# Optimization experiments

Measured on AMD Instinct MI355X. Metric: run time of the kernel, lower is better.

Reference implementation:

```python
import jax, jax.numpy as jnp
import numpy as np

BS, T, FIN, FOUT = 8, 1024, 512, 512
ALPHA = 0.1      # leaky relu slope
T_K = 3          # t_ksize (odd); temporal band radius = T_K // 2
S_K = 4          # s_ksize semantic topk
NEG_INF = -9e15


def setup_inputs() -> dict:
    key = jax.random.key(0)
    k1, k2, k3, k4 = jax.random.split(key, 4)
    # xavier-uniform-ish scales (gain 1.414)
    w_lim = 1.414 * np.sqrt(6.0 / (FIN + FOUT))
    a_lim = 1.414 * np.sqrt(6.0 / (2 * FOUT + 1))
    return {
        "x_a": jax.random.normal(k1, (BS, T, FIN), jnp.float32),
        "x_v": jax.random.normal(k2, (BS, T, FIN), jnp.float32),
        "W": jax.random.uniform(k3, (FIN, FOUT), jnp.float32, -w_lim, w_lim),
        "a": jax.random.uniform(k4, (2 * FOUT, 1), jnp.float32, -a_lim, a_lim),
    }


def _temporal_mask(t):
    # tem_adj[i,j] = 1 iff |i-j| <= T_K//2 and i, j on the same side of t-0.5
    idx = jnp.arange(2 * t)
    same_side = (idx[:, None] >= t) == (idx[None, :] >= t)
    band = jnp.abs(idx[:, None] - idx[None, :]) <= (T_K // 2)
    return band & same_side  # (2t, 2t) bool


def _semantic_block_mask(x, k):
    # x: (bs, t, d). Top-k neighbors by negative squared euclidean distance.
    inner = 2.0 * jnp.einsum("btd,bsd->bts", x, x)
    sq = jnp.sum(x * x, axis=-1, keepdims=True)  # (bs, t, 1)
    pd = -(sq - inner + jnp.swapaxes(sq, -1, -2))  # (bs, t, t)
    _, idx = jax.lax.top_k(pd, k)  # (bs, t, k)
    bs, t = x.shape[0], x.shape[1]
    b_ix = jnp.arange(bs)[:, None, None]
    r_ix = jnp.arange(t)[None, :, None]
    return jnp.zeros((bs, t, t), bool).at[b_ix, r_ix, idx].set(True)


def reference(x_a, x_v, W, a):
    bs, t, _ = x_a.shape
    h = jnp.concatenate([x_a, x_v], axis=1)          # (bs, 2t, FIN)
    Wh = h @ W                                        # (bs, 2t, FOUT)

    # additive GAT score: e = leakyrelu(Wh a1 + (Wh a2)^T)
    Wh1 = Wh @ a[:FOUT]                               # (bs, 2t, 1)
    Wh2 = Wh @ a[FOUT:]                               # (bs, 2t, 1)
    e = Wh1 + jnp.swapaxes(Wh2, -1, -2)               # (bs, 2t, 2t)
    e = jnp.where(e > 0, e, ALPHA * e)                # leaky relu

    # adjacency: temporal band + semantic topk within aa / vv blocks
    tem = _temporal_mask(t)                           # (2t, 2t)
    sem_aa = _semantic_block_mask(Wh[:, :t], S_K)     # (bs, t, t)
    sem_vv = _semantic_block_mask(Wh[:, t:], S_K)     # (bs, t, t)
    zb = jnp.zeros((bs, t, t), bool)
    sem = jnp.concatenate([
        jnp.concatenate([sem_aa, zb], axis=-1),
        jnp.concatenate([zb, sem_vv], axis=-1),
    ], axis=1)                                        # (bs, 2t, 2t)
    mask = tem[None] | sem

    attention = jax.nn.softmax(jnp.where(mask, e, NEG_INF), axis=-1)
    h_prime = jax.nn.elu(attention @ Wh)              # (bs, 2t, FOUT)
    return h_prime[:, :t], h_prime[:, t:]
```

## Files before the change

### kernel.cpp

```cpp
#include <hip/hip_runtime.h>
#include <math.h>

#define T_ 1024
#define BS_ 8
#define D_ 512
#define NROWS_ (BS_*2*T_)
#define ALPHA_ 0.1f

typedef _Float16 f16;
typedef _Float16 f16x8 __attribute__((ext_vector_type(8)));
typedef _Float16 f16x4 __attribute__((ext_vector_type(4)));
typedef float f32x4 __attribute__((ext_vector_type(4)));

#define MFMA16(A,B,C) __builtin_amdgcn_mfma_f32_16x16x32_f16((A),(B),(C),0,0,0)

__device__ __forceinline__ void gl16(const void* g, void* l) {
    __builtin_amdgcn_global_load_lds(
        (const __attribute__((address_space(1))) unsigned int*)g,
        (__attribute__((address_space(3))) unsigned int*)l, 16, 0, 0);
}

__device__ __forceinline__ unsigned sortable(float f) {
    unsigned u = __float_as_uint(f);
    return u ^ ((u & 0x80000000u) ? 0xFFFFFFFFu : 0x80000000u);
}
__device__ __forceinline__ unsigned pack_key(float s, int col) {
    return (sortable(s) & 0xFFFFFC00u) | (unsigned)(1023 - col);
}

#define INSK4(K, X) { \
    bool g3 = (X) > K[3], g2 = (X) > K[2], g1 = (X) > K[1], g0 = (X) > K[0]; \
    K[3] = g2 ? K[2] : (g3 ? (X) : K[3]); \
    K[2] = g1 ? K[1] : (g2 ? (X) : K[2]); \
    K[1] = g0 ? K[0] : (g1 ? (X) : K[1]); \
    K[0] = g0 ? (X) : K[0]; }

#define INSK8(K, X) { \
    bool h7=(X)>K[7],h6=(X)>K[6],h5=(X)>K[5],h4=(X)>K[4]; \
    bool h3=(X)>K[3],h2=(X)>K[2],h1=(X)>K[1],h0=(X)>K[0]; \
    K[7]=h6?K[6]:(h7?(X):K[7]); K[6]=h5?K[5]:(h6?(X):K[6]); \
    K[5]=h4?K[4]:(h5?(X):K[5]); K[4]=h3?K[3]:(h4?(X):K[4]); \
    K[3]=h2?K[2]:(h3?(X):K[3]); K[2]=h1?K[1]:(h2?(X):K[2]); \
    K[1]=h0?K[0]:(h1?(X):K[1]); K[0]=h0?(X):K[0]; }

#define CEU(a,b) { unsigned mx_ = (a) > (b) ? (a) : (b); \
    unsigned mn_ = (a) > (b) ? (b) : (a); (a) = mx_; (b) = mn_; }

#define MERGE8(K, MSK) { \
    unsigned b0=__shfl_xor(K[0],MSK), b1=__shfl_xor(K[1],MSK), \
             b2=__shfl_xor(K[2],MSK), b3=__shfl_xor(K[3],MSK), \
             b4=__shfl_xor(K[4],MSK), b5=__shfl_xor(K[5],MSK), \
             b6=__shfl_xor(K[6],MSK), b7=__shfl_xor(K[7],MSK); \
    K[0]=K[0]>b7?K[0]:b7; K[1]=K[1]>b6?K[1]:b6; \
    K[2]=K[2]>b5?K[2]:b5; K[3]=K[3]>b4?K[3]:b4; \
    K[4]=K[4]>b3?K[4]:b3; K[5]=K[5]>b2?K[5]:b2; \
    K[6]=K[6]>b1?K[6]:b1; K[7]=K[7]>b0?K[7]:b0; \
    CEU(K[0],K[4]); CEU(K[1],K[5]); CEU(K[2],K[6]); CEU(K[3],K[7]); \
    CEU(K[0],K[2]); CEU(K[1],K[3]); CEU(K[4],K[6]); CEU(K[5],K[7]); \
    CEU(K[0],K[1]); CEU(K[2],K[3]); CEU(K[4],K[5]); CEU(K[6],K[7]); }

#define BETTER(x,xi,v,vi) ((x) > (v) || ((x) == (v) && (xi) < (vi)))
#define INS4T(TV,TI,X,ID) { \
    bool g3 = BETTER(X,ID,TV[3],TI[3]), g2 = BETTER(X,ID,TV[2],TI[2]); \
    bool g1 = BETTER(X,ID,TV[1],TI[1]), g0 = BETTER(X,ID,TV[0],TI[0]); \
    TV[3] = g2 ? TV[2] : (g3 ? (X) : TV[3]); TI[3] = g2 ? TI[2] : (g3 ? (ID) : TI[3]); \
    TV[2] = g1 ? TV[1] : (g2 ? (X) : TV[2]); TI[2] = g1 ? TI[1] : (g2 ? (ID) : TI[2]); \
    TV[1] = g0 ? TV[0] : (g1 ? (X) : TV[1]); TI[1] = g0 ? TI[0] : (g1 ? (ID) : TI[1]); \
    TV[0] = g0 ? (X) : TV[0]; TI[0] = g0 ? (ID) : TI[0]; }

__global__ __launch_bounds__(256) void k_splitW(
    const float* __restrict__ W, f16* __restrict__ WTh, f16* __restrict__ WTl)
{
    __shared__ float tile[64][65];
    const int tid = threadIdx.x;
    const int tk = (blockIdx.x >> 3) << 6, tn = (blockIdx.x & 7) << 6;
    const int r0 = tid >> 4, c4 = (tid & 15) << 2;

    #pragma unroll
    for (int rr = 0; rr < 4; ++rr) {
        int k = r0 + (rr << 4);
        float4 v = *(const float4*)(W + (size_t)(tk + k) * D_ + tn + c4);
        tile[k][c4+0] = v.x; tile[k][c4+1] = v.y;
        tile[k][c4+2] = v.z; tile[k][c4+3] = v.w;
    }
    __syncthreads();
    #pragma unroll
    for (int rr = 0; rr < 4; ++rr) {
        int n = r0 + (rr << 4);
        f16x4 h, l;
        #pragma unroll
        for (int i = 0; i < 4; ++i) {
            float x = tile[c4 + i][n];
            f16 hh = (f16)x; h[i] = hh; l[i] = (f16)(x - (float)hh);
        }
        *(f16x4*)(WTh + (size_t)(tn + n) * D_ + tk + c4) = h;
        *(f16x4*)(WTl + (size_t)(tn + n) * D_ + tk + c4) = l;
    }
}

__global__ __launch_bounds__(512, 2) void k_gemm_wh(
    const float* __restrict__ xa, const float* __restrict__ xv,
    const f16* __restrict__ WTh, const f16* __restrict__ WTl,
    const float* __restrict__ a,
    f16* __restrict__ Whh, f16* __restrict__ Whl,
    float* __restrict__ Wh1, float* __restrict__ Wh2, float* __restrict__ sq)
{
    __shared__ __align__(16) unsigned char smem[135168];

    const int tid  = threadIdx.x;
    const int w    = tid >> 6;
    const int wr   = w >> 2, wc = w & 3;
    const int lane = tid & 63;
    const int l15  = lane & 15;
    const int g    = lane >> 4;
    const int r8   = lane >> 3;
    const int k7   = lane & 7;
    const int sw2  = ((k7 ^ r8) << 4);
    const int q0x  = ((g ^ (lane & 7)) << 4);
    const int rowbase = blockIdx.x << 6;

    if (tid < 256)
        *(float4*)(smem + 131072 + (tid << 4)) = *(const float4*)(a + (tid << 2));

    const int qp = rowbase >> 10;
    const float* xsrc = ((qp & 1) ? xv : xa)
                      + (size_t)((qp >> 1) * 1024 + (rowbase & 1023)) * D_;
    const int arow = (wr << 5) + l15;

    const char* WThB = (const char*)WTh;
    const char* WTlB = (const char*)WTl;

    const int bo0 = (((wc << 6) +  0 + l15) << 7) + q0x;
    const int bo1 = (((wc << 6) + 16 + l15) << 7) + q0x;
    const int bo2 = (((wc << 6) + 32 + l15) << 7) + q0x;
    const int bo3 = (((wc << 6) + 48 + l15) << 7) + q0x;

    #define STAGE_B(ct_, kc_, buf_) { \
        size_t gB_ = ((size_t)(((ct_) << 8) + (w << 5) + r8) << 10) + ((kc_) << 7) + sw2; \
        int ldsB_ = (buf_) * 65536 + (w << 12) + (lane << 4); \
        _Pragma("unroll") \
        for (int j_ = 0; j_ < 4; ++j_) { \
            gl16(WThB + gB_, smem + ldsB_); \
            gl16(WTlB + gB_, smem + 32768 + ldsB_); \
            gB_ += (size_t)8 << 10; ldsB_ += 1024; } }

    #define LOAD_A(dst_, kc_) { \
        _Pragma("unroll") \
        for (int r_ = 0; r_ < 2; ++r_) { \
            const float* p_ = xsrc + (size_t)(arow + (r_ << 4)) * D_ + ((kc_) << 6) + (g << 3); \
            dst_[(r_ << 2) + 0] = *(const float4*)(p_); \
            dst_[(r_ << 2) + 1] = *(const float4*)(p_ + 4); \
            dst_[(r_ << 2) + 2] = *(const float4*)(p_ + 32); \
            dst_[(r_ << 2) + 3] = *(const float4*)(p_ + 36); } }

    #define CONV_A(src_) { \
        _Pragma("unroll") \
        for (int r_ = 0; r_ < 2; ++r_) \
        _Pragma("unroll") \
        for (int s_ = 0; s_ < 2; ++s_) { \
            float4 v0_ = src_[(r_ << 2) + (s_ << 1)]; \
            float4 v1_ = src_[(r_ << 2) + (s_ << 1) + 1]; \
            float xs_[8] = {v0_.x,v0_.y,v0_.z,v0_.w,v1_.x,v1_.y,v1_.z,v1_.w}; \
            f16x8 h_, l_; \
            _Pragma("unroll") \
            for (int e_ = 0; e_ < 8; ++e_) { \
                f16 hh_ = (f16)xs_[e_]; h_[e_] = hh_; l_[e_] = (f16)(xs_[e_] - (float)hh_); } \
            AH[r_][s_] = h_; AL[r_][s_] = l_; } }

    f32x4 acc[2][2][4];
    #pragma unroll
    for (int ct = 0; ct < 2; ++ct)
        #pragma unroll
        for (int m = 0; m < 2; ++m)
            #pragma unroll
            for (int c = 0; c < 4; ++c) acc[ct][m][c] = (f32x4){0.f,0.f,0.f,0.f};

    float4 aR[8];
    f16x8 AH[2][2], AL[2][2];

    LOAD_A(aR, 0);
    STAGE_B(0, 0, 0);

    #pragma unroll
    for (int t = 0; t < 16; ++t) {
        const int kc = t >> 1, ct = t & 1, bufb = (t & 1) * 65536;
        __syncthreads();
        if (t < 15) STAGE_B((t + 1) & 1, (t + 1) >> 1, (t + 1) & 1);
        if (ct == 0) { CONV_A(aR); }
        else if (kc < 7) { LOAD_A(aR, kc + 1); }

        #pragma unroll
        for (int s = 0; s < 2; ++s) {
            const int sx = s << 6;
            f16x8 bh0 = *(const f16x8*)(smem + bufb + (bo0 ^ sx));
            f16x8 bh1 = *(const f16x8*)(smem + bufb + (bo1 ^ sx));
            f16x8 bh2 = *(const f16x8*)(smem + bufb + (bo2 ^ sx));
            f16x8 bh3 = *(const f16x8*)(smem + bufb + (bo3 ^ sx));
            f16x8 bl0 = *(const f16x8*)(smem + bufb + 32768 + (bo0 ^ sx));
            f16x8 bl1 = *(const f16x8*)(smem + bufb + 32768 + (bo1 ^ sx));
            f16x8 bl2 = *(const f16x8*)(smem + bufb + 32768 + (bo2 ^ sx));
            f16x8 bl3 = *(const f16x8*)(smem + bufb + 32768 + (bo3 ^ sx));

            acc[ct][0][0] = MFMA16(AH[0][s], bh0, acc[ct][0][0]);
            acc[ct][0][1] = MFMA16(AH[0][s], bh1, acc[ct][0][1]);
            acc[ct][0][2] = MFMA16(AH[0][s], bh2, acc[ct][0][2]);
            acc[ct][0][3] = MFMA16(AH[0][s], bh3, acc[ct][0][3]);
            acc[ct][1][0] = MFMA16(AH[1][s], bh0, acc[ct][1][0]);
            acc[ct][1][1] = MFMA16(AH[1][s], bh1, acc[ct][1][1]);
            acc[ct][1][2] = MFMA16(AH[1][s], bh2, acc[ct][1][2]);
            acc[ct][1][3] = MFMA16(AH[1][s], bh3, acc[ct][1][3]);
            acc[ct][0][0] = MFMA16(AL[0][s], bh0, acc[ct][0][0]);
            acc[ct][0][1] = MFMA16(AL[0][s], bh1, acc[ct][0][1]);
            acc[ct][0][2] = MFMA16(AL[0][s], bh2, acc[ct][0][2]);
            acc[ct][0][3] = MFMA16(AL[0][s], bh3, acc[ct][0][3]);
            acc[ct][1][0] = MFMA16(AL[1][s], bh0, acc[ct][1][0]);
            acc[ct][1][1] = MFMA16(AL[1][s], bh1, acc[ct][1][1]);
            acc[ct][1][2] = MFMA16(AL[1][s], bh2, acc[ct][1][2]);
            acc[ct][1][3] = MFMA16(AL[1][s], bh3, acc[ct][1][3]);
            acc[ct][0][0] = MFMA16(AH[0][s], bl0, acc[ct][0][0]);
            acc[ct][0][1] = MFMA16(AH[0][s], bl1, acc[ct][0][1]);
            acc[ct][0][2] = MFMA16(AH[0][s], bl2, acc[ct][0][2]);
            acc[ct][0][3] = MFMA16(AH[0][s], bl3, acc[ct][0][3]);
            acc[ct][1][0] = MFMA16(AH[1][s], bl0, acc[ct][1][0]);
            acc[ct][1][1] = MFMA16(AH[1][s], bl1, acc[ct][1][1]);
            acc[ct][1][2] = MFMA16(AH[1][s], bl2, acc[ct][1][2]);
            acc[ct][1][3] = MFMA16(AH[1][s], bl3, acc[ct][1][3]);
        }
    }
    #undef STAGE_B
    #undef LOAD_A
    #undef CONV_A

    __syncthreads();

    float st1[8], st2[8], stq[8];
    #pragma unroll
    for (int s = 0; s < 8; ++s) { st1[s] = 0.f; st2[s] = 0.f; stq[s] = 0.f; }

    #pragma unroll
    for (int ct = 0; ct < 2; ++ct)
        #pragma unroll
        for (int c = 0; c < 4; ++c) {
            const int col = (ct << 8) + (wc << 6) + (c << 4) + l15;
            const float a1 = *(const float*)(smem + 131072 + (col << 2));
            const float a2 = *(const float*)(smem + 131072 + 2048 + (col << 2));
            #pragma unroll
            for (int m = 0; m < 2; ++m)
                #pragma unroll
                for (int j = 0; j < 4; ++j) {
                    const float v = acc[ct][m][c][j];
                    const int slot = (m << 2) + j;
                    st1[slot] = fmaf(v, a1, st1[slot]);
                    st2[slot] = fmaf(v, a2, st2[slot]);
                    stq[slot] = fmaf(v, v,  stq[slot]);
                    f16 h = (f16)v; f16 l = (f16)(v - (float)h);
                    const size_t off = (size_t)(rowbase + (wr << 5) + (m << 4) + (g << 2) + j) * D_ + col;
                    Whh[off] = h; Whl[off] = l;
                }
        }

    #pragma unroll
    for (int mask = 1; mask < 16; mask <<= 1)
        #pragma unroll
        for (int s = 0; s < 8; ++s) {
            st1[s] += __shfl_xor(st1[s], mask);
            st2[s] += __shfl_xor(st2[s], mask);
            stq[s] += __shfl_xor(stq[s], mask);
        }
    if (l15 == 0) {
        #pragma unroll
        for (int s = 0; s < 8; ++s) {
            const int rl = (wr << 5) + ((s >> 2) << 4) + (g << 2) + (s & 3);
            float* sp = (float*)smem + ((rl << 2) + wc) * 3;
            sp[0] = st1[s]; sp[1] = st2[s]; sp[2] = stq[s];
        }
    }
    __syncthreads();
    if (tid < 64) {
        float s1 = 0.f, s2 = 0.f, s3 = 0.f;
        #pragma unroll
        for (int wv = 0; wv < 4; ++wv) {
            const float* sp = (const float*)smem + ((tid << 2) + wv) * 3;
            s1 += sp[0]; s2 += sp[1]; s3 += sp[2];
        }
        Wh1[rowbase + tid] = s1; Wh2[rowbase + tid] = s2; sq[rowbase + tid] = s3;
    }
}

__global__ __launch_bounds__(512, 1) void k_gram_topk8(
    const f16* __restrict__ Whh, const float* __restrict__ sq,
    int* __restrict__ topk8)
{
    __shared__ __align__(16) unsigned char smem[81920];

    const int bid = blockIdx.x;
    const int swz = ((bid & 7) << 5) + (bid >> 3);
    const int p   = swz >> 4;
    const int rt  = swz & 15;
    const int rowbase  = (p << 10) + (rt << 6);
    const int colPanel = p << 10;

    const int tid  = threadIdx.x;
    const int w    = tid >> 6;
    const int wr   = w >> 2, wc = w & 3;
    const int lane = tid & 63;
    const int l15  = lane & 15;
    const int g    = lane >> 4;
    const int r8   = lane >> 3;
    const int k7   = lane & 7;
    const int sw2  = ((k7 ^ r8) << 4);
    const int q0x  = ((g ^ (lane & 7)) << 4);

    const int rowA = tid >> 3;
    const int k7A  = tid & 7;
    const int aswz = ((k7A ^ (rowA & 7)) << 4);

    const char* WB = (const char*)Whh;

    const int aoff0 = 32768 + (((wr << 5) +  0 + l15) << 7) + q0x;
    const int aoff1 = 32768 + (((wr << 5) + 16 + l15) << 7) + q0x;
    const int boff0 = (((wc << 6) +  0 + l15) << 7) + q0x;
    const int boff1 = (((wc << 6) + 16 + l15) << 7) + q0x;
    const int boff2 = (((wc << 6) + 32 + l15) << 7) + q0x;
    const int boff3 = (((wc << 6) + 48 + l15) << 7) + q0x;

    f32x4 acc[2][4];
    #pragma unroll
    for (int m = 0; m < 2; ++m)
        #pragma unroll
        for (int c = 0; c < 4; ++c) acc[m][c] = (f32x4){0.f,0.f,0.f,0.f};

    unsigned k4[8][4];
    #pragma unroll
    for (int s = 0; s < 8; ++s)
        #pragma unroll
        for (int q = 0; q < 4; ++q) k4[s][q] = 0u;

    #define STAGE_G(t) { \
        const int ct_ = (t) >> 3, kc_ = (t) & 7; \
        const int bufb_ = ((t) & 1) * 40960; \
        size_t gB_ = ((size_t)(colPanel + (ct_ << 8) + (w << 5) + r8) << 10) + (kc_ << 7) + sw2; \
        int ldsB_ = bufb_ + (w << 12) + (lane << 4); \
        _Pragma("unroll") \
        for (int j_ = 0; j_ < 4; ++j_) { \
            gl16(WB + gB_, smem + ldsB_); \
            gB_ += (size_t)8 << 10; ldsB_ += 1024; \
        } \
        size_t gA_ = ((size_t)(rowbase + rowA) << 10) + (kc_ << 7) + aswz; \
        gl16(WB + gA_, smem + bufb_ + 32768 + (tid << 4)); \
    }

    STAGE_G(0);

    for (int t = 0; t < 32; ++t) {
        __syncthreads();
        if (t < 31) STAGE_G(t + 1);
        const int bufb = (t & 1) * 40960;

        #pragma unroll
        for (int s = 0; s < 2; ++s) {
            const int sx = s << 6;
            f16x8 a0 = *(const f16x8*)(smem + bufb + (aoff0 ^ sx));
            f16x8 a1 = *(const f16x8*)(smem + bufb + (aoff1 ^ sx));
            f16x8 b0 = *(const f16x8*)(smem + bufb + (boff0 ^ sx));
            f16x8 b1 = *(const f16x8*)(smem + bufb + (boff1 ^ sx));
            f16x8 b2 = *(const f16x8*)(smem + bufb + (boff2 ^ sx));
            f16x8 b3 = *(const f16x8*)(smem + bufb + (boff3 ^ sx));
            acc[0][0] = MFMA16(a0, b0, acc[0][0]);
            acc[0][1] = MFMA16(a0, b1, acc[0][1]);
            acc[0][2] = MFMA16(a0, b2, acc[0][2]);
            acc[0][3] = MFMA16(a0, b3, acc[0][3]);
            acc[1][0] = MFMA16(a1, b0, acc[1][0]);
            acc[1][1] = MFMA16(a1, b1, acc[1][1]);
            acc[1][2] = MFMA16(a1, b2, acc[1][2]);
            acc[1][3] = MFMA16(a1, b3, acc[1][3]);
        }

        if ((t & 7) == 7) {
            const int ct = t >> 3;
            #pragma unroll
            for (int c = 0; c < 4; ++c) {
                const int cl = (ct << 8) + (wc << 6) + (c << 4) + l15;
                const float sqc = sq[colPanel + cl];
                #pragma unroll
                for (int m = 0; m < 2; ++m)
                    #pragma unroll
                    for (int j = 0; j < 4; ++j) {
                        float sc = fmaf(2.f, acc[m][c][j], -sqc);
                        unsigned key = pack_key(sc, cl);
                        INSK4(k4[(m << 2) + j], key);
                    }
                acc[0][c] = (f32x4){0.f,0.f,0.f,0.f};
                acc[1][c] = (f32x4){0.f,0.f,0.f,0.f};
            }
        }
    }

    unsigned k8[8][8];
    #pragma unroll
    for (int s = 0; s < 8; ++s) {
        #pragma unroll
        for (int q = 0; q < 4; ++q) { k8[s][q] = k4[s][q]; k8[s][4 + q] = 0u; }
    }
    #pragma unroll
    for (int msk = 1; msk < 16; msk <<= 1) {
        #pragma unroll
        for (int s = 0; s < 8; ++s) { MERGE8(k8[s], msk); }
    }

    if (l15 == 0) {
        #pragma unroll
        for (int s = 0; s < 8; ++s) {
            const int row_local = ((s >> 2) << 4) + (g << 2) + (s & 3);
            const int off = ((((wr << 5) + row_local) << 2) + wc) << 5;
            *(uint4*)(smem + off)      = make_uint4(k8[s][0], k8[s][1], k8[s][2], k8[s][3]);
            *(uint4*)(smem + off + 16) = make_uint4(k8[s][4], k8[s][5], k8[s][6], k8[s][7]);
        }
    }
    __syncthreads();
    if (tid < 64) {
        const unsigned* bp = (const unsigned*)smem + (tid << 5);
        unsigned kk[8];
        #pragma unroll
        for (int s = 0; s < 8; ++s) kk[s] = bp[s];
        #pragma unroll
        for (int wv = 1; wv < 4; ++wv)
            #pragma unroll
            for (int s = 0; s < 8; ++s) { unsigned x = bp[(wv << 3) + s]; INSK8(kk, x); }
        #pragma unroll
        for (int s = 0; s < 8; ++s)
            topk8[(((size_t)(rowbase + tid)) << 3) + s] = 1023 - (int)(kk[s] & 1023u);
    }
    #undef STAGE_G
}

__global__ __launch_bounds__(256) void k_rescore_agg(
    const f16* __restrict__ Whh, const f16* __restrict__ Whl,
    const float* __restrict__ Wh1, const float* __restrict__ Wh2,
    const float* __restrict__ sq, const int* __restrict__ topk8,
    float* __restrict__ out)
{
    const int bid = blockIdx.x;
    const int swz = ((bid & 7) << 9) + (bid >> 3);
    const int tid  = threadIdx.x;
    const int lane = tid & 63;
    const int r    = (swz << 2) + (tid >> 6);
    const int p    = r >> 10;
    const int i    = r & 1023;
    const int rb   = p << 10;

    const size_t ro = (size_t)r * D_ + (lane << 3);
    f16x8 ah = *(const f16x8*)(Whh + ro);
    f16x8 al = *(const f16x8*)(Whl + ro);
    float av[8];
    #pragma unroll
    for (int e = 0; e < 8; ++e) av[e] = (float)ah[e] + (float)al[e];

    int cid[8];
    {
        int4 t0 = *(const int4*)(topk8 + ((size_t)r << 3));
        int4 t1 = *(const int4*)(topk8 + ((size_t)r << 3) + 4);
        cid[0]=t0.x; cid[1]=t0.y; cid[2]=t0.z; cid[3]=t0.w;
        cid[4]=t1.x; cid[5]=t1.y; cid[6]=t1.z; cid[7]=t1.w;
    }

    float dp[8];
    #pragma unroll
    for (int c = 0; c < 8; ++c) {
        const size_t co = (size_t)(rb + cid[c]) * D_ + (lane << 3);
        f16x8 bh = *(const f16x8*)(Whh + co);
        f16x8 bl = *(const f16x8*)(Whl + co);
        float s = 0.f;
        #pragma unroll
        for (int e = 0; e < 8; ++e)
            s = fmaf(av[e], (float)bh[e] + (float)bl[e], s);
        dp[c] = s;
    }
    #pragma unroll
    for (int off = 32; off > 0; off >>= 1)
        #pragma unroll
        for (int c = 0; c < 8; ++c) dp[c] += __shfl_xor(dp[c], off);

    float tv[4] = {-3.4e38f,-3.4e38f,-3.4e38f,-3.4e38f};
    int   ti[4] = {0x7FFFFFFF,0x7FFFFFFF,0x7FFFFFFF,0x7FFFFFFF};
    #pragma unroll
    for (int c = 0; c < 8; ++c) {
        float sc = fmaf(2.f, dp[c], -sq[rb + cid[c]]);
        INS4T(tv, ti, sc, cid[c]);
    }

    const int  tM = i - 1, tC = i, tP = i + 1;
    const bool vM = (i > 0), vP = (i < T_ - 1);
    const int s0 = ti[0], s1 = ti[1], s2 = ti[2], s3 = ti[3];

    bool u0 = !((vM && s0 == tM) || (s0 == tC) || (vP && s0 == tP));
    bool u1 = !((vM && s1 == tM) || (s1 == tC) || (vP && s1 == tP));
    bool u2 = !((vM && s2 == tM) || (s2 == tC) || (vP && s2 == tP));
    bool u3 = !((vM && s3 == tM) || (s3 == tC) || (vP && s3 == tP));

    int  ci[7] = { vM ? tM : 0, tC, vP ? tP : 0, s0, s1, s2, s3 };
    bool cv[7] = { vM, true, vP, u0, u1, u2, u3 };

    const float e1 = Wh1[r];
    float ev[7];
    float m = -3.4e38f;
    #pragma unroll
    for (int q = 0; q < 7; ++q) {
        float e = e1 + Wh2[rb + ci[q]];
        e = (e > 0.f) ? e : ALPHA_ * e;
        e = cv[q] ? e : -3.4e38f;
        ev[q] = e;
        m = fmaxf(m, e);
    }
    float wsum = 0.f;
    #pragma unroll
    for (int q = 0; q < 7; ++q) {
        float wq = cv[q] ? expf(ev[q] - m) : 0.f;
        ev[q] = wq;
        wsum += wq;
    }
    #pragma unroll
    for (int q = 0; q < 7; ++q) ev[q] /= wsum;

    float A[8] = {0.f,0.f,0.f,0.f,0.f,0.f,0.f,0.f};
    #pragma unroll
    for (int q = 0; q < 7; ++q) {
        if (ev[q] > 0.f) {
            const float wq = ev[q];
            const size_t qo = (size_t)(rb + ci[q]) * D_ + (lane << 3);
            f16x8 vh = *(const f16x8*)(Whh + qo);
            f16x8 vl = *(const f16x8*)(Whl + qo);
            #pragma unroll
            for (int e = 0; e < 8; ++e)
                A[e] = fmaf(wq, (float)vh[e] + (float)vl[e], A[e]);
        }
    }
    #pragma unroll
    for (int e = 0; e < 8; ++e)
        A[e] = (A[e] > 0.f) ? A[e] : expm1f(A[e]);

    const int blk = p & 1, b = p >> 1;
    float* dst = out + (size_t)blk * ((size_t)BS_ * T_ * D_)
               + ((size_t)((b << 10) + i)) * D_ + (lane << 3);
    *(float4*)(dst)     = make_float4(A[0], A[1], A[2], A[3]);
    *(float4*)(dst + 4) = make_float4(A[4], A[5], A[6], A[7]);
}

extern "C" void kernel_launch(void* const* d_in, const int* in_sizes, int n_in,
                              void* d_out, int out_size, void* d_ws, size_t ws_size,
                              hipStream_t stream)
{
    const float* xa = (const float*)d_in[0];
    const float* xv = (const float*)d_in[1];
    const float* W  = (const float*)d_in[2];
    const float* a  = (const float*)d_in[3];
    float* out = (float*)d_out;

    f16* Whh    = (f16*)d_ws;
    f16* Whl    = Whh + (size_t)NROWS_ * D_;
    f16* WTh    = Whl + (size_t)NROWS_ * D_;
    f16* WTl    = WTh + (size_t)D_ * D_;
    float* Wh1  = (float*)(WTl + (size_t)D_ * D_);
    float* Wh2  = Wh1 + NROWS_;
    float* sq   = Wh2 + NROWS_;
    int* topk8  = (int*)(sq + NROWS_);

    k_splitW     <<<dim3(64),   dim3(256), 0, stream>>>(W, WTh, WTl);
    k_gemm_wh    <<<dim3(256),  dim3(512), 0, stream>>>(xa, xv, WTh, WTl, a, Whh, Whl, Wh1, Wh2, sq);
    k_gram_topk8 <<<dim3(256),  dim3(512), 0, stream>>>(Whh, sq, topk8);
    k_rescore_agg<<<dim3(4096), dim3(256), 0, stream>>>(Whh, Whl, Wh1, Wh2, sq, topk8, out);
}
```

Baseline: 126.6 us.

## Split Wh GEMM across column halves and use fdot2 in rescore dot products

The Wh GEMM now splits each 64-row tile across two blocks, each covering half of the output columns. This doubles the grid to 512 blocks, halves shared memory, and raises the occupancy hint, with a block-index swizzle applied. Per-row partial stats (Wh1, Wh2, sq) go to a scratch buffer and are summed by a new small k_stats kernel, which adds a launch and duplicates the A-tile loads and conversion across blocks. The rescore kernel replaces the float-upconverted dot product with packed f16 fdot2 instructions over the hi/lo split, dropping the lo*lo term, which slightly changes precision.

Result: slower. 131.6 us (+3.9%).

```diff
diff --git a/kernel.cpp b/kernel.cpp
--- a/kernel.cpp
+++ b/kernel.cpp
@@ -10,6 +10,7 @@
 typedef _Float16 f16;
 typedef _Float16 f16x8 __attribute__((ext_vector_type(8)));
 typedef _Float16 f16x4 __attribute__((ext_vector_type(4)));
+typedef _Float16 f16x2 __attribute__((ext_vector_type(2)));
 typedef float f32x4 __attribute__((ext_vector_type(4)));
 
 #define MFMA16(A,B,C) __builtin_amdgcn_mfma_f32_16x16x32_f16((A),(B),(C),0,0,0)
@@ -18,6 +19,27 @@
     __builtin_amdgcn_global_load_lds(
         (const __attribute__((address_space(1))) unsigned int*)g,
         (__attribute__((address_space(3))) unsigned int*)l, 16, 0, 0);
+}
+
+#if __has_builtin(__builtin_amdgcn_fdot2)
+__device__ __forceinline__ float fdot2p(f16x2 a, f16x2 b, float c) {
+    return __builtin_amdgcn_fdot2(a, b, c, false);
+}
+#else
+__device__ __forceinline__ float fdot2p(f16x2 a, f16x2 b, float c) {
+    return fmaf((float)a[1], (float)b[1], fmaf((float)a[0], (float)b[0], c));
+}
+#endif
+
+__device__ __forceinline__ float fdot8(const f16x8 a, const f16x8 b, float s) {
+    #pragma unroll
+    for (int q = 0; q < 4; ++q) {
+        f16x2 aa, bb;
+        aa[0] = a[2*q]; aa[1] = a[2*q+1];
+        bb[0] = b[2*q]; bb[1] = b[2*q+1];
+        s = fdot2p(aa, bb, s);
+    }
+    return s;
 }
 
 __device__ __forceinline__ unsigned sortable(float f) {
@@ -98,14 +120,14 @@
     }
 }
 
-__global__ __launch_bounds__(512, 2) void k_gemm_wh(
+__global__ __launch_bounds__(512, 4) void k_gemm_wh(
     const float* __restrict__ xa, const float* __restrict__ xv,
     const f16* __restrict__ WTh, const f16* __restrict__ WTl,
     const float* __restrict__ a,
     f16* __restrict__ Whh, f16* __restrict__ Whl,
-    float* __restrict__ Wh1, float* __restrict__ Wh2, float* __restrict__ sq)
+    float* __restrict__ stP)
 {
-    __shared__ __align__(16) unsigned char smem[135168];
+    __shared__ __align__(16) unsigned char smem[69632];
 
     const int tid  = threadIdx.x;
     const int w    = tid >> 6;
@@ -113,14 +135,13 @@
     const int lane = tid & 63;
     const int l15  = lane & 15;
     const int g    = lane >> 4;
-    const int r8   = lane >> 3;
-    const int k7   = lane & 7;
-    const int sw2  = ((k7 ^ r8) << 4);
-    const int q0x  = ((g ^ (lane & 7)) << 4);
-    const int rowbase = blockIdx.x << 6;
+    const int bid  = blockIdx.x;
+    const int swz  = ((bid & 7) << 6) + (bid >> 3);
+    const int rowbase = (swz >> 1) << 6;
+    const int nt   = swz & 1;
 
     if (tid < 256)
-        *(float4*)(smem + 131072 + (tid << 4)) = *(const float4*)(a + (tid << 2));
+        *(float4*)(smem + 65536 + (tid << 4)) = *(const float4*)(a + (tid << 2));
 
     const int qp = rowbase >> 10;
     const float* xsrc = ((qp & 1) ? xv : xa)
@@ -130,19 +151,21 @@
     const char* WThB = (const char*)WTh;
     const char* WTlB = (const char*)WTl;
 
-    const int bo0 = (((wc << 6) +  0 + l15) << 7) + q0x;
-    const int bo1 = (((wc << 6) + 16 + l15) << 7) + q0x;
-    const int bo2 = (((wc << 6) + 32 + l15) << 7) + q0x;
-    const int bo3 = (((wc << 6) + 48 + l15) << 7) + q0x;
-
-    #define STAGE_B(ct_, kc_, buf_) { \
-        size_t gB_ = ((size_t)(((ct_) << 8) + (w << 5) + r8) << 10) + ((kc_) << 7) + sw2; \
-        int ldsB_ = (buf_) * 65536 + (w << 12) + (lane << 4); \
-        _Pragma("unroll") \
-        for (int j_ = 0; j_ < 4; ++j_) { \
-            gl16(WThB + gB_, smem + ldsB_); \
-            gl16(WTlB + gB_, smem + 32768 + ldsB_); \
-            gB_ += (size_t)8 << 10; ldsB_ += 1024; } }
+    const int col0 = tid >> 3;
+    const int j80  = (tid & 7) ^ (col0 & 7);
+
+    const int bo0 = (((wc << 5) +  0 + l15) << 7) + ((g ^ (l15 & 7)) << 4);
+    const int bo1 = (((wc << 5) + 16 + l15) << 7) + ((g ^ (l15 & 7)) << 4);
+
+    #define STAGE_B(t_) { \
+        const int kc_ = (t_) >> 1, cq_ = (t_) & 1; \
+        const int bufb_ = ((t_) & 1) << 15; \
+        const size_t g0_ = ((size_t)((nt << 8) + (cq_ << 7) + col0) << 10) + ((size_t)kc_ << 7) + (j80 << 4); \
+        const size_t g1_ = g0_ + ((size_t)64 << 10); \
+        gl16(WThB + g0_, smem + bufb_ + (tid << 4)); \
+        gl16(WThB + g1_, smem + bufb_ + ((tid + 512) << 4)); \
+        gl16(WTlB + g0_, smem + bufb_ + 16384 + (tid << 4)); \
+        gl16(WTlB + g1_, smem + bufb_ + 16384 + ((tid + 512) << 4)); }
 
     #define LOAD_A(dst_, kc_) { \
         _Pragma("unroll") \
@@ -167,26 +190,26 @@
                 f16 hh_ = (f16)xs_[e_]; h_[e_] = hh_; l_[e_] = (f16)(xs_[e_] - (float)hh_); } \
             AH[r_][s_] = h_; AL[r_][s_] = l_; } }
 
-    f32x4 acc[2][2][4];
-    #pragma unroll
-    for (int ct = 0; ct < 2; ++ct)
+    f32x4 acc[2][2][2];
+    #pragma unroll
+    for (int cq = 0; cq < 2; ++cq)
         #pragma unroll
         for (int m = 0; m < 2; ++m)
             #pragma unroll
-            for (int c = 0; c < 4; ++c) acc[ct][m][c] = (f32x4){0.f,0.f,0.f,0.f};
+            for (int c = 0; c < 2; ++c) acc[cq][m][c] = (f32x4){0.f,0.f,0.f,0.f};
 
     float4 aR[8];
     f16x8 AH[2][2], AL[2][2];
 
     LOAD_A(aR, 0);
-    STAGE_B(0, 0, 0);
+    STAGE_B(0);
 
     #pragma unroll
     for (int t = 0; t < 16; ++t) {
-        const int kc = t >> 1, ct = t & 1, bufb = (t & 1) * 65536;
+        const int kc = t >> 1, cq = t & 1, bufb = (t & 1) << 15;
         __syncthreads();
-        if (t < 15) STAGE_B((t + 1) & 1, (t + 1) >> 1, (t + 1) & 1);
-        if (ct == 0) { CONV_A(aR); }
+        if (t < 15) STAGE_B(t + 1);
+        if (cq == 0) { CONV_A(aR); }
         else if (kc < 7) { LOAD_A(aR, kc + 1); }
 
         #pragma unroll
@@ -194,37 +217,21 @@
             const int sx = s << 6;
             f16x8 bh0 = *(const f16x8*)(smem + bufb + (bo0 ^ sx));
             f16x8 bh1 = *(const f16x8*)(smem + bufb + (bo1 ^ sx));
-            f16x8 bh2 = *(const f16x8*)(smem + bufb + (bo2 ^ sx));
-            f16x8 bh3 = *(const f16x8*)(smem + bufb + (bo3 ^ sx));
-            f16x8 bl0 = *(const f16x8*)(smem + bufb + 32768 + (bo0 ^ sx));
-            f16x8 bl1 = *(const f16x8*)(smem + bufb + 32768 + (bo1 ^ sx));
-            f16x8 bl2 = *(const f16x8*)(smem + bufb + 32768 + (bo2 ^ sx));
-            f16x8 bl3 = *(const f16x8*)(smem + bufb + 32768 + (bo3 ^ sx));
-
-            acc[ct][0][0] = MFMA16(AH[0][s], bh0, acc[ct][0][0]);
-            acc[ct][0][1] = MFMA16(AH[0][s], bh1, acc[ct][0][1]);
-            acc[ct][0][2] = MFMA16(AH[0][s], bh2, acc[ct][0][2]);
-            acc[ct][0][3] = MFMA16(AH[0][s], bh3, acc[ct][0][3]);
-            acc[ct][1][0] = MFMA16(AH[1][s], bh0, acc[ct][1][0]);
-            acc[ct][1][1] = MFMA16(AH[1][s], bh1, acc[ct][1][1]);
-            acc[ct][1][2] = MFMA16(AH[1][s], bh2, acc[ct][1][2]);
-            acc[ct][1][3] = MFMA16(AH[1][s], bh3, acc[ct][1][3]);
-            acc[ct][0][0] = MFMA16(AL[0][s], bh0, acc[ct][0][0]);
-            acc[ct][0][1] = MFMA16(AL[0][s], bh1, acc[ct][0][1]);
-            acc[ct][0][2] = MFMA16(AL[0][s], bh2, acc[ct][0][2]);
-            acc[ct][0][3] = MFMA16(AL[0][s], bh3, acc[ct][0][3]);
-            acc[ct][1][0] = MFMA16(AL[1][s], bh0, acc[ct][1][0]);
-            acc[ct][1][1] = MFMA16(AL[1][s], bh1, acc[ct][1][1]);
-            acc[ct][1][2] = MFMA16(AL[1][s], bh2, acc[ct][1][2]);
-            acc[ct][1][3] = MFMA16(AL[1][s], bh3, acc[ct][1][3]);
-            acc[ct][0][0] = MFMA16(AH[0][s], bl0, acc[ct][0][0]);
-            acc[ct][0][1] = MFMA16(AH[0][s], bl1, acc[ct][0][1]);
-            acc[ct][0][2] = MFMA16(AH[0][s], bl2, acc[ct][0][2]);
-            acc[ct][0][3] = MFMA16(AH[0][s], bl3, acc[ct][0][3]);
-            acc[ct][1][0] = MFMA16(AH[1][s], bl0, acc[ct][1][0]);
-            acc[ct][1][1] = MFMA16(AH[1][s], bl1, acc[ct][1][1]);
-            acc[ct][1][2] = MFMA16(AH[1][s], bl2, acc[ct][1][2]);
-            acc[ct][1][3] = MFMA16(AH[1][s], bl3, acc[ct][1][3]);
+            f16x8 bl0 = *(const f16x8*)(smem + bufb + 16384 + (bo0 ^ sx));
+            f16x8 bl1 = *(const f16x8*)(smem + bufb + 16384 + (bo1 ^ sx));
+
+            acc[cq][0][0] = MFMA16(AH[0][s], bh0, acc[cq][0][0]);
+            acc[cq][0][1] = MFMA16(AH[0][s], bh1, acc[cq][0][1]);
+            acc[cq][1][0] = MFMA16(AH[1][s], bh0, acc[cq][1][0]);
+            acc[cq][1][1] = MFMA16(AH[1][s], bh1, acc[cq][1][1]);
+            acc[cq][0][0] = MFMA16(AL[0][s], bh0, acc[cq][0][0]);
+            acc[cq][0][1] = MFMA16(AL[0][s], bh1, acc[cq][0][1]);
+            acc[cq][1][0] = MFMA16(AL[1][s], bh0, acc[cq][1][0]);
+            acc[cq][1][1] = MFMA16(AL[1][s], bh1, acc[cq][1][1]);
+            acc[cq][0][0] = MFMA16(AH[0][s], bl0, acc[cq][0][0]);
+            acc[cq][0][1] = MFMA16(AH[0][s], bl1, acc[cq][0][1]);
+            acc[cq][1][0] = MFMA16(AH[1][s], bl0, acc[cq][1][0]);
+            acc[cq][1][1] = MFMA16(AH[1][s], bl1, acc[cq][1][1]);
         }
     }
     #undef STAGE_B
@@ -238,17 +245,17 @@
     for (int s = 0; s < 8; ++s) { st1[s] = 0.f; st2[s] = 0.f; stq[s] = 0.f; }
 
     #pragma unroll
-    for (int ct = 0; ct < 2; ++ct)
-        #pragma unroll
-        for (int c = 0; c < 4; ++c) {
-            const int col = (ct << 8) + (wc << 6) + (c << 4) + l15;
-            const float a1 = *(const float*)(smem + 131072 + (col << 2));
-            const float a2 = *(const float*)(smem + 131072 + 2048 + (col << 2));
+    for (int cq = 0; cq < 2; ++cq)
+        #pragma unroll
+        for (int c = 0; c < 2; ++c) {
+            const int col = (nt << 8) + (cq << 7) + (wc << 5) + (c << 4) + l15;
+            const float a1 = *(const float*)(smem + 65536 + (col << 2));
+            const float a2 = *(const float*)(smem + 65536 + 2048 + (col << 2));
             #pragma unroll
             for (int m = 0; m < 2; ++m)
                 #pragma unroll
                 for (int j = 0; j < 4; ++j) {
-                    const float v = acc[ct][m][c][j];
+                    const float v = acc[cq][m][c][j];
                     const int slot = (m << 2) + j;
                     st1[slot] = fmaf(v, a1, st1[slot]);
                     st2[slot] = fmaf(v, a2, st2[slot]);
@@ -283,8 +290,23 @@
             const float* sp = (const float*)smem + ((tid << 2) + wv) * 3;
             s1 += sp[0]; s2 += sp[1]; s3 += sp[2];
         }
-        Wh1[rowbase + tid] = s1; Wh2[rowbase + tid] = s2; sq[rowbase + tid] = s3;
-    }
+        float* base = stP + (size_t)nt * 3 * NROWS_;
+        base[rowbase + tid]              = s1;
+        base[NROWS_ + rowbase + tid]     = s2;
+        base[2 * NROWS_ + rowbase + tid] = s3;
+    }
+}
+
+__global__ __launch_bounds__(256) void k_stats(
+    const float* __restrict__ stP, float* __restrict__ Wh1,
+    float* __restrict__ Wh2, float* __restrict__ sq)
+{
+    const int i = (blockIdx.x << 8) + threadIdx.x;
+    const float* p0 = stP;
+    const float* p1 = stP + 3 * NROWS_;
+    Wh1[i] = p0[i] + p1[i];
+    Wh2[i] = p0[NROWS_ + i] + p1[NROWS_ + i];
+    sq[i]  = p0[2 * NROWS_ + i] + p1[2 * NROWS_ + i];
 }
 
 __global__ __launch_bounds__(512, 1) void k_gram_topk8(
@@ -452,9 +474,6 @@
     const size_t ro = (size_t)r * D_ + (lane << 3);
     f16x8 ah = *(const f16x8*)(Whh + ro);
     f16x8 al = *(const f16x8*)(Whl + ro);
-    float av[8];
-    #pragma unroll
-    for (int e = 0; e < 8; ++e) av[e] = (float)ah[e] + (float)al[e];
 
     int cid[8];
     {
@@ -471,9 +490,9 @@
         f16x8 bh = *(const f16x8*)(Whh + co);
         f16x8 bl = *(const f16x8*)(Whl + co);
         float s = 0.f;
-        #pragma unroll
-        for (int e = 0; e < 8; ++e)
-            s = fmaf(av[e], (float)bh[e] + (float)bl[e], s);
+        s = fdot8(ah, bh, s);
+        s = fdot8(ah, bl, s);
+        s = fdot8(al, bh, s);
         dp[c] = s;
     }
     #pragma unroll
@@ -531,8 +550,9 @@
             f16x8 vh = *(const f16x8*)(Whh + qo);
             f16x8 vl = *(const f16x8*)(Whl + qo);
             #pragma unroll
-            for (int e = 0; e < 8; ++e)
-                A[e] = fmaf(wq, (float)vh[e] + (float)vl[e], A[e]);
+            for (int e = 0; e < 8; ++e) A[e] = fmaf(wq, (float)vh[e], A[e]);
+            #pragma unroll
+            for (int e = 0; e < 8; ++e) A[e] = fmaf(wq, (float)vl[e], A[e]);
         }
     }
     #pragma unroll
@@ -564,9 +584,11 @@
     float* Wh2  = Wh1 + NROWS_;
     float* sq   = Wh2 + NROWS_;
     int* topk8  = (int*)(sq + NROWS_);
+    float* stP  = (float*)(topk8 + ((size_t)NROWS_ << 3));
 
     k_splitW     <<<dim3(64),   dim3(256), 0, stream>>>(W, WTh, WTl);
-    k_gemm_wh    <<<dim3(256),  dim3(512), 0, stream>>>(xa, xv, WTh, WTl, a, Whh, Whl, Wh1, Wh2, sq);
+    k_gemm_wh    <<<dim3(512),  dim3(512), 0, stream>>>(xa, xv, WTh, WTl, a, Whh, Whl, stP);
+    k_stats      <<<dim3(64),   dim3(256), 0, stream>>>(stP, Wh1, Wh2, sq);
     k_gram_topk8 <<<dim3(256),  dim3(512), 0, stream>>>(Whh, sq, topk8);
     k_rescore_agg<<<dim3(4096), dim3(256), 0, stream>>>(Whh, Whl, Wh1, Wh2, sq, topk8, out);
 }
```
